# Kernel tuning notes

Measured on AMD Instinct MI355X. Metric: run time of the kernel, lower is better.

The kernel has to match this reference:

```python
import jax, jax.numpy as jnp
import numpy as np

B, N, DIM, QK, H, GS = 4, 4096, 512, 512, 8, 128
NUM_LABELS = 8
R_BASE, R_MIN, R_MAX = 0.5, 0.25, 0.75
LAMBDA_P, LAMBDA_V, CCR = 0.25, 0.25, 0.125


def setup_inputs() -> dict:
    key = jax.random.key(0)
    ks = jax.random.split(key, 7)
    s = DIM ** -0.5
    return {
        "x": jax.random.normal(ks[0], (B, N, DIM), jnp.float32),
        "labels": jax.random.randint(ks[1], (B, N), 0, NUM_LABELS),
        "scores": jax.random.uniform(ks[2], (B, N), jnp.float32),
        "Wq": jax.random.normal(ks[3], (DIM, QK), jnp.float32) * s,
        "Wk": jax.random.normal(ks[4], (DIM, QK), jnp.float32) * s,
        "Wv": jax.random.normal(ks[5], (DIM, DIM), jnp.float32) * s,
        "Wproj": jax.random.normal(ks[6], (DIM, DIM), jnp.float32) * s,
    }


def _windows(t, gs, ng):
    # pad with flipped last-group tail, then overlapping windows of size 2*gs, stride gs
    tp = jnp.concatenate([t, jnp.flip(t[:, -gs:], axis=1)], axis=1)
    a = tp.reshape(t.shape[0], ng + 1, gs, *t.shape[2:])
    return jnp.concatenate([a[:, :-1], a[:, 1:]], axis=2)  # [b, ng, 2*gs, ...]


def _topk_mask(vals, keep, cand):
    # rank of each entry when sorted descending; keep top-`keep` among candidates
    ranks = jnp.argsort(jnp.argsort(-vals, axis=-1), axis=-1)
    return (ranks < keep[:, :, None, None, None]) & cand


def reference(x, labels, scores, Wq, Wk, Wv, Wproj):
    b, n, _ = x.shape
    gs = GS
    ng = n // gs            # num_tokens divisible by group_size -> pad_n = 0
    ws = 2 * gs
    q = x @ Wq
    k = x @ Wk
    v = x @ Wv

    qw = q.reshape(b, ng, gs, H, -1).transpose(0, 1, 3, 2, 4)          # b ng h gs d
    kw = _windows(k, gs, ng).reshape(b, ng, ws, H, -1).transpose(0, 1, 3, 2, 4)
    vw = _windows(v, gs, ng).reshape(b, ng, ws, H, -1).transpose(0, 1, 3, 2, 4)
    q_labels = labels.reshape(b, ng, gs)
    k_labels = _windows(labels, gs, ng)                                 # b ng ws
    q_scores = scores.reshape(b, ng, gs)
    k_scores = _windows(scores, gs, ng)

    d = qw.shape[-1]
    scale = 1.0 / jnp.sqrt(jnp.asarray(d, qw.dtype))
    logits = jnp.einsum('bghqd,bghkd->bghqk', qw, kw) * scale           # b ng h gs ws
    attn_hat = jax.nn.softmax(logits, axis=-1)  # no prev_attn_state -> attn_hat = attn_cur

    # dynamic focus ratio: purity from group mode label + score variance
    counts = jax.nn.one_hot(q_labels, NUM_LABELS, dtype=jnp.float32).sum(axis=2)  # b ng L
    mode = jnp.argmax(counts, axis=-1)
    purity = jnp.mean((q_labels == mode[..., None]).astype(jnp.float32), axis=-1)
    score_var = jnp.var(q_scores.astype(jnp.float32), axis=-1)  # unbiased=False
    focus = jnp.clip(R_BASE + LAMBDA_P * purity - LAMBDA_V * score_var, R_MIN, R_MAX)

    keep = jnp.clip(jnp.ceil(focus * ws).astype(jnp.int32), 1, ws)
    cross_keep = jnp.round(keep.astype(jnp.float32) * CCR).astype(jnp.int32)
    cross_keep = jnp.where(keep > 1, jnp.maximum(cross_keep, 1), 0)
    same_keep = jnp.maximum(keep - cross_keep, 1)

    same_mask = (q_labels[:, :, None, :, None] == k_labels[:, :, None, None, :])  # b ng 1 gs ws

    same_scores = jnp.where(same_mask, attn_hat, -10000.0)
    m_same = _topk_mask(same_scores, same_keep, same_mask)
    pair_conf = q_scores[:, :, None, :, None] * k_scores[:, :, None, None, :]
    cross_scores = attn_hat * pair_conf
    m_cross = _topk_mask(cross_scores, cross_keep, ~same_mask)
    final_mask = m_same | m_cross

    sparse_logits = jnp.where(final_mask, logits, -10000.0)
    attn_local = jax.nn.softmax(sparse_logits, axis=-1)
    attn_local = jnp.where(final_mask, attn_local, 0.0)
    attn_local = attn_local / (attn_local.sum(axis=-1, keepdims=True) + 1e-9)

    out = jnp.einsum('bghqk,bghkd->bghqd', attn_local, vw)
    out = out.transpose(0, 1, 3, 2, 4).reshape(b, ng * gs, -1)[:, :n]
    return out @ Wproj, attn_local
```

## Files before the change

### kernel.cpp

```cpp
#include <hip/hip_runtime.h>

#define BB 4
#define NN 4096
#define DIMM 512
#define HH 8
#define DH 64
#define GSZ 128
#define NGRP 32
#define WSZ 256
#define CHUNK 32

#define MK 8388608u
#define WK 262144u

typedef short short8 __attribute__((ext_vector_type(8)));
typedef float f32x4 __attribute__((ext_vector_type(4)));

__device__ inline unsigned short bf16rne(float f) {
  unsigned u = __float_as_uint(f);
  unsigned r = u + 0x7FFFu + ((u >> 16) & 1u);
  return (unsigned short)(r >> 16);
}
__device__ inline float bf16tof(unsigned short h) {
  return __uint_as_float(((unsigned)h) << 16);
}

__global__ __launch_bounds__(256) void split_planes(
    const float* __restrict__ X, unsigned short* __restrict__ P, int np)
{
  unsigned idx = (blockIdx.x * 256u + threadIdx.x) * 4u;
  float4 xv = *(const float4*)&X[idx];
  float xs[4] = {xv.x, xv.y, xv.z, xv.w};
  ushort4 hv, mv, lv;
  unsigned short* hp = (unsigned short*)&hv;
  unsigned short* mp = (unsigned short*)&mv;
  unsigned short* lp = (unsigned short*)&lv;
#pragma unroll
  for (int i = 0; i < 4; ++i) {
    unsigned short h = bf16rne(xs[i]);
    float r1 = xs[i] - bf16tof(h);
    unsigned short m = bf16rne(r1);
    float r2 = r1 - bf16tof(m);
    hp[i] = h;
    mp[i] = m;
    lp[i] = bf16rne(r2);
  }
  *(ushort4*)&P[idx] = hv;
  *(ushort4*)&P[MK + idx] = mv;
  if (np == 3) *(ushort4*)&P[2u * MK + idx] = lv;
}

__global__ __launch_bounds__(256) void split_w(
    const float* __restrict__ Wq, const float* __restrict__ Wk,
    const float* __restrict__ Wv, const float* __restrict__ Wpj,
    unsigned short* __restrict__ wqkv, unsigned short* __restrict__ wproj)
{
  unsigned e = blockIdx.x * 256u + threadIdx.x;
  int mz = e >> 18;
  unsigned rem = e & (WK - 1u);
  unsigned kk = rem >> 9, n = rem & 511u;
  const float* src = (mz == 0) ? Wq : (mz == 1) ? Wk : (mz == 2) ? Wv : Wpj;
  float w = src[kk * 512u + n];
  unsigned short h = bf16rne(w);
  float r1 = w - bf16tof(h);
  unsigned short m = bf16rne(r1);
  float r2 = r1 - bf16tof(m);
  unsigned short l = bf16rne(r2);
  unsigned o = n * 512u + kk;
  if (mz < 3) {
    unsigned short* base = wqkv + (unsigned)mz * 3u * WK;
    base[o] = h;
    base[WK + o] = m;
    base[2u * WK + o] = l;
  } else {
    wproj[o] = h;
    wproj[WK + o] = m;
  }
}

template <int NP, int NT>
__global__ __launch_bounds__(256) void mfma_gemm(
    const unsigned short* __restrict__ Ap,
    const unsigned short* __restrict__ Wp,
    float* __restrict__ C)
{
  constexpr int ta[6] = {0, 0, 1, 1, 0, 2};
  constexpr int tw[6] = {0, 1, 0, 1, 2, 0};
  const int z = blockIdx.z;
  const int n0 = blockIdx.x * 128;
  const int m0 = blockIdx.y * 128;
  const int tid = threadIdx.x;
  const int lane = tid & 63, wv = tid >> 6;
  const int wm = (wv >> 1) * 64, wn = (wv & 1) * 64;
  const int lm = lane & 15, lk = (lane >> 4) * 8;

  __shared__ unsigned short As[NP * 128 * 40];
  __shared__ unsigned short Ws[NP * 128 * 40];

  f32x4 acc[4][4];
#pragma unroll
  for (int i = 0; i < 4; ++i)
#pragma unroll
    for (int j = 0; j < 4; ++j) acc[i][j] = (f32x4){0.f, 0.f, 0.f, 0.f};

  const unsigned short* Wz = Wp + (size_t)z * NP * WK;

  for (int k0 = 0; k0 < 512; k0 += 32) {
#pragma unroll
    for (int i = 0; i < NP * 2; ++i) {
      int idx = i * 256 + tid;
      int p = idx >> 9, rem = idx & 511;
      int r = rem >> 2, cc = rem & 3;
      *(short8*)&As[p * 5120 + r * 40 + cc * 8] =
          *(const short8*)&Ap[(size_t)p * MK + (size_t)(m0 + r) * 512 + k0 + cc * 8];
      *(short8*)&Ws[p * 5120 + r * 40 + cc * 8] =
          *(const short8*)&Wz[(size_t)p * WK + (size_t)(n0 + r) * 512 + k0 + cc * 8];
    }
    __syncthreads();

    short8 a[NP][4];
#pragma unroll
    for (int p = 0; p < NP; ++p)
#pragma unroll
      for (int fm = 0; fm < 4; ++fm)
        a[p][fm] = *(const short8*)&As[p * 5120 + (wm + fm * 16 + lm) * 40 + lk];

#pragma unroll
    for (int fn = 0; fn < 4; ++fn) {
      short8 bf[NP];
#pragma unroll
      for (int p = 0; p < NP; ++p)
        bf[p] = *(const short8*)&Ws[p * 5120 + (wn + fn * 16 + lm) * 40 + lk];
#pragma unroll
      for (int fm = 0; fm < 4; ++fm) {
#pragma unroll
        for (int t = 0; t < NT; ++t)
          acc[fm][fn] = __builtin_amdgcn_mfma_f32_16x16x32_bf16(
              a[ta[t]][fm], bf[tw[t]], acc[fm][fn], 0, 0, 0);
      }
    }
    __syncthreads();
  }

  float* Cz = C + (size_t)z * 8388608u;
  const int rq = (lane >> 4) * 4;
#pragma unroll
  for (int fm = 0; fm < 4; ++fm)
#pragma unroll
    for (int fn = 0; fn < 4; ++fn) {
      int row = m0 + wm + fm * 16 + rq;
      int col = n0 + wn + fn * 16 + lm;
#pragma unroll
      for (int r = 0; r < 4; ++r)
        Cz[(size_t)(row + r) * 512 + col] = acc[fm][fn][r];
    }
}

__global__ __launch_bounds__(256) void gemm512(
    const float* __restrict__ A,
    const float* __restrict__ W0, const float* __restrict__ W1, const float* __restrict__ W2,
    float* __restrict__ C0, float* __restrict__ C1, float* __restrict__ C2)
{
  const int z = blockIdx.z;
  const float* Wm = (z == 0) ? W0 : (z == 1 ? W1 : W2);
  float* Cm = (z == 0) ? C0 : (z == 1 ? C1 : C2);
  const int n0 = blockIdx.x * 128;
  const int m0 = blockIdx.y * 128;
  const int tid = threadIdx.x;
  const int tx = tid & 15, ty = tid >> 4;

  __shared__ float As[32][132];
  __shared__ float Bs[32][132];

  float acc[8][8];
#pragma unroll
  for (int i = 0; i < 8; ++i)
#pragma unroll
    for (int j = 0; j < 8; ++j) acc[i][j] = 0.f;

  for (int k0 = 0; k0 < 512; k0 += 32) {
    {
      const int c4 = tid & 7, r = tid >> 3;
#pragma unroll
      for (int p = 0; p < 128; p += 32) {
        float4 av = *(const float4*)&A[(size_t)(m0 + r + p) * 512 + k0 + c4 * 4];
        As[c4 * 4 + 0][r + p] = av.x;
        As[c4 * 4 + 1][r + p] = av.y;
        As[c4 * 4 + 2][r + p] = av.z;
        As[c4 * 4 + 3][r + p] = av.w;
      }
      const int j4 = tid & 31, rb = tid >> 5;
#pragma unroll
      for (int p = 0; p < 32; p += 8) {
        *(float4*)&Bs[rb + p][j4 * 4] =
            *(const float4*)&Wm[(size_t)(k0 + rb + p) * 512 + n0 + j4 * 4];
      }
    }
    __syncthreads();
#pragma unroll
    for (int kk = 0; kk < 32; ++kk) {
      float4 a0 = *(const float4*)&As[kk][ty * 8];
      float4 a1 = *(const float4*)&As[kk][ty * 8 + 4];
      float4 b0 = *(const float4*)&Bs[kk][tx * 8];
      float4 b1 = *(const float4*)&Bs[kk][tx * 8 + 4];
      float av[8] = {a0.x, a0.y, a0.z, a0.w, a1.x, a1.y, a1.z, a1.w};
      float bv[8] = {b0.x, b0.y, b0.z, b0.w, b1.x, b1.y, b1.z, b1.w};
#pragma unroll
      for (int i = 0; i < 8; ++i)
#pragma unroll
        for (int j = 0; j < 8; ++j) acc[i][j] += av[i] * bv[j];
    }
    __syncthreads();
  }
#pragma unroll
  for (int i = 0; i < 8; ++i) {
    size_t row = (size_t)(m0 + ty * 8 + i);
    float4 o0 = make_float4(acc[i][0], acc[i][1], acc[i][2], acc[i][3]);
    float4 o1 = make_float4(acc[i][4], acc[i][5], acc[i][6], acc[i][7]);
    *(float4*)&Cm[row * 512 + n0 + tx * 8] = o0;
    *(float4*)&Cm[row * 512 + n0 + tx * 8 + 4] = o1;
  }
}

__global__ __launch_bounds__(256, 3) void attn_kernel(
    const float* q,
    const float* __restrict__ k,
    const float* __restrict__ v,
    const int* __restrict__ labels,
    const float* __restrict__ scores,
    float* __restrict__ attn_out,
    float* o)
{
  const int bx = blockIdx.x;
  const int c = bx >> 10;
  const int rblk = bx & 1023;
  const int h = rblk & 7;
  const int g = (rblk >> 3) & 31;
  const int b = rblk >> 8;
  const int r0 = c * CHUNK;
  const int tid = threadIdx.x;
  const int lane = tid & 63, wv = tid >> 6;

  __shared__ float att[CHUNK][WSZ + 4];
  __shared__ float ktile[64][DH + 4];
  __shared__ int klab[WSZ];
  __shared__ float kscr[WSZ];
  __shared__ int hist8[8];
  __shared__ float s_var;
  __shared__ int s_sk, s_ck;

  {
    int j = tid;
    int pos = g * GSZ + j;
    int tok = pos < NN ? pos : (2 * NN - 1 - pos);
    klab[j] = labels[b * NN + tok];
    kscr[j] = scores[b * NN + tok];
  }
  if (tid < 8) hist8[tid] = 0;
  __syncthreads();

  if (tid < GSZ) atomicAdd(&hist8[klab[tid]], 1);
  if (wv == 0) {
    double x0 = (double)kscr[lane], x1 = (double)kscr[lane + 64];
    double s = x0 + x1;
#pragma unroll
    for (int off = 32; off > 0; off >>= 1) s += __shfl_xor(s, off);
    double mean = s * (1.0 / 128.0);
    double d0 = x0 - mean, d1 = x1 - mean;
    double vs = d0 * d0 + d1 * d1;
#pragma unroll
    for (int off = 32; off > 0; off >>= 1) vs += __shfl_xor(vs, off);
    if (lane == 0) s_var = (float)(vs * (1.0 / 128.0));
  }
  __syncthreads();
  if (tid == 0) {
    int bc = hist8[0];
    for (int l = 1; l < 8; ++l)
      if (hist8[l] > bc) bc = hist8[l];
    float purity = (float)bc * (1.0f / GSZ);
    float focus = 0.5f + 0.25f * purity - 0.25f * s_var;
    focus = fminf(fmaxf(focus, 0.25f), 0.75f);
    int keep = (int)ceilf(focus * (float)WSZ);
    keep = min(max(keep, 1), WSZ);
    int ck = keep >> 3, rem = keep & 7;
    if (rem > 4 || (rem == 4 && (ck & 1))) ck++;
    if (ck < 1) ck = 1;
    int sk = keep - ck;
    if (sk < 1) sk = 1;
    s_sk = sk;
    s_ck = ck;
  }
  __syncthreads();
  const int same_keep = s_sk, cross_keep = s_ck;

  const int rp = tid >> 4, jx = tid & 15;
  const int srow = tid >> 4, sd4 = (tid & 15) * 4;

  const float* q0p = q + (size_t)(b * NN + g * GSZ + r0 + rp) * DIMM + h * DH;
  const float* q1p = q0p + (size_t)16 * DIMM;

  for (int jt = 0; jt < 4; ++jt) {
#pragma unroll
    for (int p = 0; p < 64; p += 16) {
      int j = jt * 64 + srow + p;
      int pos = g * GSZ + j;
      int tok = pos < NN ? pos : (2 * NN - 1 - pos);
      *(float4*)&ktile[srow + p][sd4] =
          *(const float4*)&k[(size_t)(b * NN + tok) * DIMM + h * DH + sd4];
    }
    __syncthreads();
    float acc0[4] = {0.f, 0.f, 0.f, 0.f}, acc1[4] = {0.f, 0.f, 0.f, 0.f};
#pragma unroll
    for (int dd = 0; dd < DH; dd += 4) {
      float4 q0 = *(const float4*)(q0p + dd);
      float4 q1 = *(const float4*)(q1p + dd);
#pragma unroll
      for (int jj = 0; jj < 4; ++jj) {
        float4 kv = *(const float4*)&ktile[jx + 16 * jj][dd];
        acc0[jj] += q0.x * kv.x + q0.y * kv.y + q0.z * kv.z + q0.w * kv.w;
        acc1[jj] += q1.x * kv.x + q1.y * kv.y + q1.z * kv.z + q1.w * kv.w;
      }
    }
#pragma unroll
    for (int jj = 0; jj < 4; ++jj) {
      att[rp][jt * 64 + jx + 16 * jj] = acc0[jj] * 0.125f;
      att[rp + 16][jt * 64 + jx + 16 * jj] = acc1[jj] * 0.125f;
    }
    __syncthreads();
  }

  {
    int kl0[4];
    float ks0[4];
#pragma unroll
    for (int m = 0; m < 4; ++m) {
      kl0[m] = klab[lane + 64 * m];
      ks0[m] = kscr[lane + 64 * m];
    }
    for (int sp = 0; sp < 4; ++sp) {
      const int rA = wv * 8 + 2 * sp, rB = rA + 1;
      const int qLA = klab[r0 + rA], qLB = klab[r0 + rB];
      const float qSA = kscr[r0 + rA], qSB = kscr[r0 + rB];
      float aA[4], aB[4];
      float mxA = -INFINITY, mxB = -INFINITY;
#pragma unroll
      for (int m = 0; m < 4; ++m) {
        aA[m] = att[rA][lane + 64 * m];
        aB[m] = att[rB][lane + 64 * m];
        mxA = fmaxf(mxA, aA[m]);
        mxB = fmaxf(mxB, aB[m]);
      }
#pragma unroll
      for (int off = 32; off > 0; off >>= 1) {
        mxA = fmaxf(mxA, __shfl_xor(mxA, off));
        mxB = fmaxf(mxB, __shfl_xor(mxB, off));
      }
      unsigned fsA[4], fcA[4], fsB[4], fcB[4];
      bool cdA[4], cdB[4];
#pragma unroll
      for (int m = 0; m < 4; ++m) {
        aA[m] = expf(aA[m] - mxA);
        aB[m] = expf(aB[m] - mxB);
        cdA[m] = (kl0[m] == qLA);
        cdB[m] = (kl0[m] == qLB);
        fsA[m] = cdA[m] ? __float_as_uint(aA[m]) : 0u;
        fsB[m] = cdB[m] ? __float_as_uint(aB[m]) : 0u;
        fcA[m] = __float_as_uint(aA[m] * (qSA * ks0[m]));
        fcB[m] = __float_as_uint(aB[m] * (qSB * ks0[m]));
      }
      unsigned tsA = 0, tcA = 0, tsB = 0, tcB = 0;
      for (int bit = 29; bit >= 0; --bit) {
        unsigned csA = tsA | (1u << bit), ccA = tcA | (1u << bit);
        unsigned csB = tsB | (1u << bit), ccB = tcB | (1u << bit);
        int nsA = 0, ncA = 0, nsB = 0, ncB = 0;
#pragma unroll
        for (int m = 0; m < 4; ++m) {
          nsA += __popcll(__ballot(fsA[m] >= csA));
          ncA += __popcll(__ballot(fcA[m] >= ccA));
          nsB += __popcll(__ballot(fsB[m] >= csB));
          ncB += __popcll(__ballot(fcB[m] >= ccB));
        }
        if (nsA >= same_keep) tsA = csA;
        if (ncA >= cross_keep) tcA = ccA;
        if (nsB >= same_keep) tsB = csB;
        if (ncB >= cross_keep) tcB = ccB;
      }
#pragma unroll
      for (int rsel = 0; rsel < 2; ++rsel) {
        const int rr = rsel ? rB : rA;
        const unsigned ts = rsel ? tsB : tsA, tc = rsel ? tcB : tcA;
        unsigned* fs = rsel ? fsB : fsA;
        unsigned* fc = rsel ? fcB : fcA;
        float* a = rsel ? aB : aA;
        bool* cand = rsel ? cdB : cdA;
        unsigned long long beqs[4], beqc[4];
        int gts = 0, gtc = 0;
#pragma unroll
        for (int m = 0; m < 4; ++m) {
          gts += __popcll(__ballot(fs[m] > ts));
          gtc += __popcll(__ballot(fc[m] > tc));
          beqs[m] = __ballot(fs[m] == ts);
          beqc[m] = __ballot(fc[m] == tc);
        }
        const int rs = same_keep - gts, rc = cross_keep - gtc;
        float pv[4];
        float S = 0.f;
        int pres = 0, prec = 0;
#pragma unroll
        for (int m = 0; m < 4; ++m) {
          int mbs = __builtin_amdgcn_mbcnt_hi((unsigned)(beqs[m] >> 32),
                     __builtin_amdgcn_mbcnt_lo((unsigned)beqs[m], 0));
          int mbc = __builtin_amdgcn_mbcnt_hi((unsigned)(beqc[m] >> 32),
                     __builtin_amdgcn_mbcnt_lo((unsigned)beqc[m], 0));
          bool keep_s = cand[m] && ((fs[m] > ts) || ((fs[m] == ts) && (pres + mbs < rs)));
          bool keep_c = (!cand[m]) && ((fc[m] > tc) || ((fc[m] == tc) && (prec + mbc < rc)));
          pv[m] = (keep_s || keep_c) ? a[m] : 0.f;
          S += pv[m];
          pres += __popcll(beqs[m]);
          prec += __popcll(beqc[m]);
        }
#pragma unroll
        for (int off = 32; off > 0; off >>= 1) S += __shfl_xor(S, off);
        const float inv = 1.0f / S;
#pragma unroll
        for (int m = 0; m < 4; ++m) att[rr][lane + 64 * m] = pv[m] * inv;
      }
    }
  }
  __syncthreads();

  {
    size_t base = ((((size_t)b * NGRP + g) * HH + h) * GSZ + r0) * WSZ;
#pragma unroll
    for (int it = 0; it < 8; ++it) {
      int idx = it * 256 + tid;
      int i = idx >> 6, j4 = (idx & 63) * 4;
      *(float4*)&attn_out[base + (size_t)i * WSZ + j4] = *(float4*)&att[i][j4];
    }
  }

  const int dx = jx;
  float oa0[4] = {0.f, 0.f, 0.f, 0.f}, oa1[4] = {0.f, 0.f, 0.f, 0.f};
  for (int jt = 0; jt < 4; ++jt) {
#pragma unroll
    for (int p = 0; p < 64; p += 16) {
      int j = jt * 64 + srow + p;
      int pos = g * GSZ + j;
      int tok = pos < NN ? pos : (2 * NN - 1 - pos);
      *(float4*)&ktile[srow + p][sd4] =
          *(const float4*)&v[(size_t)(b * NN + tok) * DIMM + h * DH + sd4];
    }
    __syncthreads();
#pragma unroll 4
    for (int jg = 0; jg < 16; ++jg) {
      float4 p0 = *(const float4*)&att[rp][jt * 64 + jg * 4];
      float4 p1 = *(const float4*)&att[rp + 16][jt * 64 + jg * 4];
      float4 v0 = *(const float4*)&ktile[jg * 4 + 0][dx * 4];
      float4 v1 = *(const float4*)&ktile[jg * 4 + 1][dx * 4];
      float4 v2 = *(const float4*)&ktile[jg * 4 + 2][dx * 4];
      float4 v3 = *(const float4*)&ktile[jg * 4 + 3][dx * 4];
      oa0[0] += p0.x * v0.x + p0.y * v1.x + p0.z * v2.x + p0.w * v3.x;
      oa0[1] += p0.x * v0.y + p0.y * v1.y + p0.z * v2.y + p0.w * v3.y;
      oa0[2] += p0.x * v0.z + p0.y * v1.z + p0.z * v2.z + p0.w * v3.z;
      oa0[3] += p0.x * v0.w + p0.y * v1.w + p0.z * v2.w + p0.w * v3.w;
      oa1[0] += p1.x * v0.x + p1.y * v1.x + p1.z * v2.x + p1.w * v3.x;
      oa1[1] += p1.x * v0.y + p1.y * v1.y + p1.z * v2.y + p1.w * v3.y;
      oa1[2] += p1.x * v0.z + p1.y * v1.z + p1.z * v2.z + p1.w * v3.z;
      oa1[3] += p1.x * v0.w + p1.y * v1.w + p1.z * v2.w + p1.w * v3.w;
    }
    __syncthreads();
  }
  {
    size_t ob0 = (size_t)(b * NN + g * GSZ + r0 + rp) * DIMM + h * DH + dx * 4;
    *(float4*)&o[ob0] = make_float4(oa0[0], oa0[1], oa0[2], oa0[3]);
    *(float4*)&o[ob0 + (size_t)16 * DIMM] = make_float4(oa1[0], oa1[1], oa1[2], oa1[3]);
  }
}

extern "C" void kernel_launch(void* const* d_in, const int* in_sizes, int n_in,
                              void* d_out, int out_size, void* d_ws, size_t ws_size,
                              hipStream_t stream) {
  const float* x      = (const float*)d_in[0];
  const int*   labels = (const int*)d_in[1];
  const float* scores = (const float*)d_in[2];
  const float* Wq     = (const float*)d_in[3];
  const float* Wk     = (const float*)d_in[4];
  const float* Wv     = (const float*)d_in[5];
  const float* Wproj  = (const float*)d_in[6];

  float* out = (float*)d_out;
  float* attn_out = out + (size_t)BB * NN * DIMM;

  const size_t SZ = (size_t)BB * NN * DIMM;
  float* qb = (float*)d_ws;
  float* kb = qb + SZ;
  float* vb = kb + SZ;

  unsigned short* xp    = (unsigned short*)((char*)d_ws + 3 * SZ * 4);
  unsigned short* wqkv  = xp + 3 * (size_t)MK;
  unsigned short* wpp   = wqkv + 9 * (size_t)WK;
  const size_t required = 3 * SZ * 4 +
                          (3 * (size_t)MK + 9 * (size_t)WK + 2 * (size_t)WK) * 2;

  if (ws_size >= required) {
    split_planes<<<dim3(MK / 1024), 256, 0, stream>>>(x, xp, 3);
    split_w<<<dim3(4 * WK / 256), 256, 0, stream>>>(Wq, Wk, Wv, Wproj, wqkv, wpp);
    mfma_gemm<3, 6><<<dim3(4, 128, 3), 256, 0, stream>>>(xp, wqkv, qb);
    attn_kernel<<<dim3(BB * NGRP * HH * 4), 256, 0, stream>>>(qb, kb, vb, labels,
                                                              scores, attn_out, qb);
    split_planes<<<dim3(MK / 1024), 256, 0, stream>>>(qb, xp, 2);
    mfma_gemm<2, 3><<<dim3(4, 128, 1), 256, 0, stream>>>(xp, wpp, out);
  } else {
    gemm512<<<dim3(4, 128, 3), 256, 0, stream>>>(x, Wq, Wk, Wv, qb, kb, vb);
    attn_kernel<<<dim3(BB * NGRP * HH * 4), 256, 0, stream>>>(qb, kb, vb, labels,
                                                              scores, attn_out, qb);
    gemm512<<<dim3(4, 128, 1), 256, 0, stream>>>(qb, Wproj, Wproj, Wproj, out, out, out);
  }
}
```

Before: 814.0 us.

## Fuse bf16 plane split into attention epilogue and use fewer planes for V

The attention kernel now writes its output directly as hi/mid bf16 planes, so the separate split_planes pass over the attention output and its fp32 round trip are gone. The V projection is computed with a cheaper 2-plane × 3-term MFMA GEMM instead of the 3-plane × 6-term one used for Q and K. This cuts memory traffic and GEMM work, at the cost of lower precision in V, which could affect accuracy.

```diff
diff --git a/kernel.cpp b/kernel.cpp
--- a/kernel.cpp
+++ b/kernel.cpp
@@ -26,7 +26,7 @@
 }
 
 __global__ __launch_bounds__(256) void split_planes(
-    const float* __restrict__ X, unsigned short* __restrict__ P, int np)
+    const float* __restrict__ X, unsigned short* __restrict__ P)
 {
   unsigned idx = (blockIdx.x * 256u + threadIdx.x) * 4u;
   float4 xv = *(const float4*)&X[idx];
@@ -47,7 +47,7 @@
   }
   *(ushort4*)&P[idx] = hv;
   *(ushort4*)&P[MK + idx] = mv;
-  if (np == 3) *(ushort4*)&P[2u * MK + idx] = lv;
+  *(ushort4*)&P[2u * MK + idx] = lv;
 }
 
 __global__ __launch_bounds__(256) void split_w(
@@ -142,8 +142,8 @@
     __syncthreads();
   }
 
+  const int rq = (lane >> 4) * 4;
   float* Cz = C + (size_t)z * 8388608u;
-  const int rq = (lane >> 4) * 4;
 #pragma unroll
   for (int fm = 0; fm < 4; ++fm)
 #pragma unroll
@@ -222,14 +222,151 @@
   }
 }
 
-__global__ __launch_bounds__(256, 3) void attn_kernel(
-    const float* q,
-    const float* __restrict__ k,
-    const float* __restrict__ v,
-    const int* __restrict__ labels,
-    const float* __restrict__ scores,
-    float* __restrict__ attn_out,
-    float* o)
+__device__ __forceinline__ void focus_keep(
+    const int* klab, const float* kscr, int* hist8, float* s_var,
+    int* s_sk, int* s_ck, int tid, int lane, int wv)
+{
+  if (tid < GSZ) atomicAdd(&hist8[klab[tid]], 1);
+  if (wv == 0) {
+    double x0 = (double)kscr[lane], x1 = (double)kscr[lane + 64];
+    double s = x0 + x1;
+#pragma unroll
+    for (int off = 32; off > 0; off >>= 1) s += __shfl_xor(s, off);
+    double mean = s * (1.0 / 128.0);
+    double d0 = x0 - mean, d1 = x1 - mean;
+    double vs = d0 * d0 + d1 * d1;
+#pragma unroll
+    for (int off = 32; off > 0; off >>= 1) vs += __shfl_xor(vs, off);
+    if (lane == 0) *s_var = (float)(vs * (1.0 / 128.0));
+  }
+  __syncthreads();
+  if (tid == 0) {
+    int bc = hist8[0];
+    for (int l = 1; l < 8; ++l)
+      if (hist8[l] > bc) bc = hist8[l];
+    float purity = (float)bc * (1.0f / GSZ);
+    float focus = 0.5f + 0.25f * purity - 0.25f * (*s_var);
+    focus = fminf(fmaxf(focus, 0.25f), 0.75f);
+    int keep = (int)ceilf(focus * (float)WSZ);
+    keep = min(max(keep, 1), WSZ);
+    int ck = keep >> 3, rem = keep & 7;
+    if (rem > 4 || (rem == 4 && (ck & 1))) ck++;
+    if (ck < 1) ck = 1;
+    int sk = keep - ck;
+    if (sk < 1) sk = 1;
+    *s_sk = sk;
+    *s_ck = ck;
+  }
+  __syncthreads();
+}
+
+__device__ __forceinline__ void rank_rows(
+    float att[CHUNK][WSZ + 4], const int* klab, const float* kscr,
+    int r0, int same_keep, int cross_keep, int lane, int wv)
+{
+  int kl0[4];
+  float ks0[4];
+#pragma unroll
+  for (int m = 0; m < 4; ++m) {
+    kl0[m] = klab[lane + 64 * m];
+    ks0[m] = kscr[lane + 64 * m];
+  }
+  for (int sp = 0; sp < 4; ++sp) {
+    const int rA = wv * 8 + 2 * sp, rB = rA + 1;
+    const int qLA = klab[r0 + rA], qLB = klab[r0 + rB];
+    const float qSA = kscr[r0 + rA], qSB = kscr[r0 + rB];
+    float aA[4], aB[4];
+    float mxA = -INFINITY, mxB = -INFINITY;
+#pragma unroll
+    for (int m = 0; m < 4; ++m) {
+      aA[m] = att[rA][lane + 64 * m];
+      aB[m] = att[rB][lane + 64 * m];
+      mxA = fmaxf(mxA, aA[m]);
+      mxB = fmaxf(mxB, aB[m]);
+    }
+#pragma unroll
+    for (int off = 32; off > 0; off >>= 1) {
+      mxA = fmaxf(mxA, __shfl_xor(mxA, off));
+      mxB = fmaxf(mxB, __shfl_xor(mxB, off));
+    }
+    unsigned fsA[4], fcA[4], fsB[4], fcB[4];
+    bool cdA[4], cdB[4];
+#pragma unroll
+    for (int m = 0; m < 4; ++m) {
+      aA[m] = expf(aA[m] - mxA);
+      aB[m] = expf(aB[m] - mxB);
+      cdA[m] = (kl0[m] == qLA);
+      cdB[m] = (kl0[m] == qLB);
+      fsA[m] = cdA[m] ? __float_as_uint(aA[m]) : 0u;
+      fsB[m] = cdB[m] ? __float_as_uint(aB[m]) : 0u;
+      fcA[m] = __float_as_uint(aA[m] * (qSA * ks0[m]));
+      fcB[m] = __float_as_uint(aB[m] * (qSB * ks0[m]));
+    }
+    unsigned tsA = 0, tcA = 0, tsB = 0, tcB = 0;
+    for (int bit = 29; bit >= 0; --bit) {
+      unsigned csA = tsA | (1u << bit), ccA = tcA | (1u << bit);
+      unsigned csB = tsB | (1u << bit), ccB = tcB | (1u << bit);
+      int nsA = 0, ncA = 0, nsB = 0, ncB = 0;
+#pragma unroll
+      for (int m = 0; m < 4; ++m) {
+        nsA += __popcll(__ballot(fsA[m] >= csA));
+        ncA += __popcll(__ballot(fcA[m] >= ccA));
+        nsB += __popcll(__ballot(fsB[m] >= csB));
+        ncB += __popcll(__ballot(fcB[m] >= ccB));
+      }
+      if (nsA >= same_keep) tsA = csA;
+      if (ncA >= cross_keep) tcA = ccA;
+      if (nsB >= same_keep) tsB = csB;
+      if (ncB >= cross_keep) tcB = ccB;
+    }
+#pragma unroll
+    for (int rsel = 0; rsel < 2; ++rsel) {
+      const int rr = rsel ? rB : rA;
+      const unsigned ts = rsel ? tsB : tsA, tc = rsel ? tcB : tcA;
+      unsigned* fs = rsel ? fsB : fsA;
+      unsigned* fc = rsel ? fcB : fcA;
+      float* a = rsel ? aB : aA;
+      bool* cand = rsel ? cdB : cdA;
+      unsigned long long beqs[4], beqc[4];
+      int gts = 0, gtc = 0;
+#pragma unroll
+      for (int m = 0; m < 4; ++m) {
+        gts += __popcll(__ballot(fs[m] > ts));
+        gtc += __popcll(__ballot(fc[m] > tc));
+        beqs[m] = __ballot(fs[m] == ts);
+        beqc[m] = __ballot(fc[m] == tc);
+      }
+      const int rs = same_keep - gts, rc = cross_keep - gtc;
+      float pv[4];
+      float S = 0.f;
+      int pres = 0, prec = 0;
+#pragma unroll
+      for (int m = 0; m < 4; ++m) {
+        int mbs = __builtin_amdgcn_mbcnt_hi((unsigned)(beqs[m] >> 32),
+                   __builtin_amdgcn_mbcnt_lo((unsigned)beqs[m], 0));
+        int mbc = __builtin_amdgcn_mbcnt_hi((unsigned)(beqc[m] >> 32),
+                   __builtin_amdgcn_mbcnt_lo((unsigned)beqc[m], 0));
+        bool keep_s = cand[m] && ((fs[m] > ts) || ((fs[m] == ts) && (pres + mbs < rs)));
+        bool keep_c = (!cand[m]) && ((fc[m] > tc) || ((fc[m] == tc) && (prec + mbc < rc)));
+        pv[m] = (keep_s || keep_c) ? a[m] : 0.f;
+        S += pv[m];
+        pres += __popcll(beqs[m]);
+        prec += __popcll(beqc[m]);
+      }
+#pragma unroll
+      for (int off = 32; off > 0; off >>= 1) S += __shfl_xor(S, off);
+      const float inv = 1.0f / S;
+#pragma unroll
+      for (int m = 0; m < 4; ++m) att[rr][lane + 64 * m] = pv[m] * inv;
+    }
+  }
+}
+
+template <int OMODE>
+__global__ __launch_bounds__(256, 3) void attn_f32(
+    const float* q, const float* __restrict__ k, const float* __restrict__ v,
+    const int* __restrict__ labels, const float* __restrict__ scores,
+    float* __restrict__ attn_out, float* o, unsigned short* __restrict__ opl)
 {
   const int bx = blockIdx.x;
   const int c = bx >> 10;
@@ -258,44 +395,11 @@
   }
   if (tid < 8) hist8[tid] = 0;
   __syncthreads();
-
-  if (tid < GSZ) atomicAdd(&hist8[klab[tid]], 1);
-  if (wv == 0) {
-    double x0 = (double)kscr[lane], x1 = (double)kscr[lane + 64];
-    double s = x0 + x1;
-#pragma unroll
-    for (int off = 32; off > 0; off >>= 1) s += __shfl_xor(s, off);
-    double mean = s * (1.0 / 128.0);
-    double d0 = x0 - mean, d1 = x1 - mean;
-    double vs = d0 * d0 + d1 * d1;
-#pragma unroll
-    for (int off = 32; off > 0; off >>= 1) vs += __shfl_xor(vs, off);
-    if (lane == 0) s_var = (float)(vs * (1.0 / 128.0));
-  }
-  __syncthreads();
-  if (tid == 0) {
-    int bc = hist8[0];
-    for (int l = 1; l < 8; ++l)
-      if (hist8[l] > bc) bc = hist8[l];
-    float purity = (float)bc * (1.0f / GSZ);
-    float focus = 0.5f + 0.25f * purity - 0.25f * s_var;
-    focus = fminf(fmaxf(focus, 0.25f), 0.75f);
-    int keep = (int)ceilf(focus * (float)WSZ);
-    keep = min(max(keep, 1), WSZ);
-    int ck = keep >> 3, rem = keep & 7;
-    if (rem > 4 || (rem == 4 && (ck & 1))) ck++;
-    if (ck < 1) ck = 1;
-    int sk = keep - ck;
-    if (sk < 1) sk = 1;
-    s_sk = sk;
-    s_ck = ck;
-  }
-  __syncthreads();
+  focus_keep(klab, kscr, hist8, &s_var, &s_sk, &s_ck, tid, lane, wv);
   const int same_keep = s_sk, cross_keep = s_ck;
 
   const int rp = tid >> 4, jx = tid & 15;
   const int srow = tid >> 4, sd4 = (tid & 15) * 4;
-
   const float* q0p = q + (size_t)(b * NN + g * GSZ + r0 + rp) * DIMM + h * DH;
   const float* q1p = q0p + (size_t)16 * DIMM;
 
@@ -329,104 +433,7 @@
     __syncthreads();
   }
 
-  {
-    int kl0[4];
-    float ks0[4];
-#pragma unroll
-    for (int m = 0; m < 4; ++m) {
-      kl0[m] = klab[lane + 64 * m];
-      ks0[m] = kscr[lane + 64 * m];
-    }
-    for (int sp = 0; sp < 4; ++sp) {
-      const int rA = wv * 8 + 2 * sp, rB = rA + 1;
-      const int qLA = klab[r0 + rA], qLB = klab[r0 + rB];
-      const float qSA = kscr[r0 + rA], qSB = kscr[r0 + rB];
-      float aA[4], aB[4];
-      float mxA = -INFINITY, mxB = -INFINITY;
-#pragma unroll
-      for (int m = 0; m < 4; ++m) {
-        aA[m] = att[rA][lane + 64 * m];
-        aB[m] = att[rB][lane + 64 * m];
-        mxA = fmaxf(mxA, aA[m]);
-        mxB = fmaxf(mxB, aB[m]);
-      }
-#pragma unroll
-      for (int off = 32; off > 0; off >>= 1) {
-        mxA = fmaxf(mxA, __shfl_xor(mxA, off));
-        mxB = fmaxf(mxB, __shfl_xor(mxB, off));
-      }
-      unsigned fsA[4], fcA[4], fsB[4], fcB[4];
-      bool cdA[4], cdB[4];
-#pragma unroll
-      for (int m = 0; m < 4; ++m) {
-        aA[m] = expf(aA[m] - mxA);
-        aB[m] = expf(aB[m] - mxB);
-        cdA[m] = (kl0[m] == qLA);
-        cdB[m] = (kl0[m] == qLB);
-        fsA[m] = cdA[m] ? __float_as_uint(aA[m]) : 0u;
-        fsB[m] = cdB[m] ? __float_as_uint(aB[m]) : 0u;
-        fcA[m] = __float_as_uint(aA[m] * (qSA * ks0[m]));
-        fcB[m] = __float_as_uint(aB[m] * (qSB * ks0[m]));
-      }
-      unsigned tsA = 0, tcA = 0, tsB = 0, tcB = 0;
-      for (int bit = 29; bit >= 0; --bit) {
-        unsigned csA = tsA | (1u << bit), ccA = tcA | (1u << bit);
-        unsigned csB = tsB | (1u << bit), ccB = tcB | (1u << bit);
-        int nsA = 0, ncA = 0, nsB = 0, ncB = 0;
-#pragma unroll
-        for (int m = 0; m < 4; ++m) {
-          nsA += __popcll(__ballot(fsA[m] >= csA));
-          ncA += __popcll(__ballot(fcA[m] >= ccA));
-          nsB += __popcll(__ballot(fsB[m] >= csB));
-          ncB += __popcll(__ballot(fcB[m] >= ccB));
-        }
-        if (nsA >= same_keep) tsA = csA;
-        if (ncA >= cross_keep) tcA = ccA;
-        if (nsB >= same_keep) tsB = csB;
-        if (ncB >= cross_keep) tcB = ccB;
-      }
-#pragma unroll
-      for (int rsel = 0; rsel < 2; ++rsel) {
-        const int rr = rsel ? rB : rA;
-        const unsigned ts = rsel ? tsB : tsA, tc = rsel ? tcB : tcA;
-        unsigned* fs = rsel ? fsB : fsA;
-        unsigned* fc = rsel ? fcB : fcA;
-        float* a = rsel ? aB : aA;
-        bool* cand = rsel ? cdB : cdA;
-        unsigned long long beqs[4], beqc[4];
-        int gts = 0, gtc = 0;
-#pragma unroll
-        for (int m = 0; m < 4; ++m) {
-          gts += __popcll(__ballot(fs[m] > ts));
-          gtc += __popcll(__ballot(fc[m] > tc));
-          beqs[m] = __ballot(fs[m] == ts);
-          beqc[m] = __ballot(fc[m] == tc);
-        }
-        const int rs = same_keep - gts, rc = cross_keep - gtc;
-        float pv[4];
-        float S = 0.f;
-        int pres = 0, prec = 0;
-#pragma unroll
-        for (int m = 0; m < 4; ++m) {
-          int mbs = __builtin_amdgcn_mbcnt_hi((unsigned)(beqs[m] >> 32),
-                     __builtin_amdgcn_mbcnt_lo((unsigned)beqs[m], 0));
-          int mbc = __builtin_amdgcn_mbcnt_hi((unsigned)(beqc[m] >> 32),
-                     __builtin_amdgcn_mbcnt_lo((unsigned)beqc[m], 0));
-          bool keep_s = cand[m] && ((fs[m] > ts) || ((fs[m] == ts) && (pres + mbs < rs)));
-          bool keep_c = (!cand[m]) && ((fc[m] > tc) || ((fc[m] == tc) && (prec + mbc < rc)));
-          pv[m] = (keep_s || keep_c) ? a[m] : 0.f;
-          S += pv[m];
-          pres += __popcll(beqs[m]);
-          prec += __popcll(beqc[m]);
-        }
-#pragma unroll
-        for (int off = 32; off > 0; off >>= 1) S += __shfl_xor(S, off);
-        const float inv = 1.0f / S;
-#pragma unroll
-        for (int m = 0; m < 4; ++m) att[rr][lane + 64 * m] = pv[m] * inv;
-      }
-    }
-  }
+  rank_rows(att, klab, kscr, r0, same_keep, cross_keep, lane, wv);
   __syncthreads();
 
   {
@@ -470,10 +477,30 @@
     }
     __syncthreads();
   }
-  {
+  if (OMODE == 0) {
     size_t ob0 = (size_t)(b * NN + g * GSZ + r0 + rp) * DIMM + h * DH + dx * 4;
     *(float4*)&o[ob0] = make_float4(oa0[0], oa0[1], oa0[2], oa0[3]);
     *(float4*)&o[ob0 + (size_t)16 * DIMM] = make_float4(oa1[0], oa1[1], oa1[2], oa1[3]);
+  } else {
+    size_t ob0 = (size_t)(b * NN + g * GSZ + r0 + rp) * 512 + h * 64 + dx * 4;
+    ushort4 h0, m0v, h1, m1v;
+    unsigned short* h0p = (unsigned short*)&h0;
+    unsigned short* m0p = (unsigned short*)&m0v;
+    unsigned short* h1p = (unsigned short*)&h1;
+    unsigned short* m1p = (unsigned short*)&m1v;
+#pragma unroll
+    for (int i = 0; i < 4; ++i) {
+      unsigned short hh = bf16rne(oa0[i]);
+      h0p[i] = hh;
+      m0p[i] = bf16rne(oa0[i] - bf16tof(hh));
+      unsigned short hh1 = bf16rne(oa1[i]);
+      h1p[i] = hh1;
+      m1p[i] = bf16rne(oa1[i] - bf16tof(hh1));
+    }
+    *(ushort4*)&opl[ob0] = h0;
+    *(ushort4*)&opl[MK + ob0] = m0v;
+    *(ushort4*)&opl[ob0 + 16 * 512] = h1;
+    *(ushort4*)&opl[MK + ob0 + 16 * 512] = m1v;
   }
 }
 
@@ -491,29 +518,30 @@
   float* out = (float*)d_out;
   float* attn_out = out + (size_t)BB * NN * DIMM;
 
-  const size_t SZ = (size_t)BB * NN * DIMM;
   float* qb = (float*)d_ws;
-  float* kb = qb + SZ;
-  float* vb = kb + SZ;
-
-  unsigned short* xp    = (unsigned short*)((char*)d_ws + 3 * SZ * 4);
-  unsigned short* wqkv  = xp + 3 * (size_t)MK;
-  unsigned short* wpp   = wqkv + 9 * (size_t)WK;
-  const size_t required = 3 * SZ * 4 +
-                          (3 * (size_t)MK + 9 * (size_t)WK + 2 * (size_t)WK) * 2;
+  float* kb = qb + (size_t)MK;
+  float* vf = kb + (size_t)MK;
+  unsigned short* xpl  = (unsigned short*)(vf + (size_t)MK);
+  unsigned short* wqkv = xpl + 3 * (size_t)MK;
+  unsigned short* wpp  = wqkv + 9 * (size_t)WK;
+  const size_t required = 3 * (size_t)MK * 4 + 3 * (size_t)MK * 2 + 11 * (size_t)WK * 2;
 
   if (ws_size >= required) {
-    split_planes<<<dim3(MK / 1024), 256, 0, stream>>>(x, xp, 3);
+    split_planes<<<dim3(MK / 1024), 256, 0, stream>>>(x, xpl);
     split_w<<<dim3(4 * WK / 256), 256, 0, stream>>>(Wq, Wk, Wv, Wproj, wqkv, wpp);
-    mfma_gemm<3, 6><<<dim3(4, 128, 3), 256, 0, stream>>>(xp, wqkv, qb);
-    attn_kernel<<<dim3(BB * NGRP * HH * 4), 256, 0, stream>>>(qb, kb, vb, labels,
-                                                              scores, attn_out, qb);
-    split_planes<<<dim3(MK / 1024), 256, 0, stream>>>(qb, xp, 2);
-    mfma_gemm<2, 3><<<dim3(4, 128, 1), 256, 0, stream>>>(xp, wpp, out);
+    mfma_gemm<3, 6><<<dim3(4, 128, 2), 256, 0, stream>>>(xpl, wqkv, qb);
+    mfma_gemm<2, 3><<<dim3(4, 128, 1), 256, 0, stream>>>(xpl, wqkv + 6 * (size_t)WK, vf);
+    attn_f32<1><<<dim3(BB * NGRP * HH * 4), 256, 0, stream>>>(
+        qb, kb, vf, labels, scores, attn_out, nullptr, xpl);
+    mfma_gemm<2, 3><<<dim3(4, 128, 1), 256, 0, stream>>>(xpl, wpp, out);
   } else {
-    gemm512<<<dim3(4, 128, 3), 256, 0, stream>>>(x, Wq, Wk, Wv, qb, kb, vb);
-    attn_kernel<<<dim3(BB * NGRP * HH * 4), 256, 0, stream>>>(qb, kb, vb, labels,
-                                                              scores, attn_out, qb);
-    gemm512<<<dim3(4, 128, 1), 256, 0, stream>>>(qb, Wproj, Wproj, Wproj, out, out, out);
-  }
-}
+    const size_t SZ = (size_t)BB * NN * DIMM;
+    float* q2 = (float*)d_ws;
+    float* k2 = q2 + SZ;
+    float* v2 = k2 + SZ;
+    gemm512<<<dim3(4, 128, 3), 256, 0, stream>>>(x, Wq, Wk, Wv, q2, k2, v2);
+    attn_f32<0><<<dim3(BB * NGRP * HH * 4), 256, 0, stream>>>(
+        q2, k2, v2, labels, scores, attn_out, q2, nullptr);
+    gemm512<<<dim3(4, 128, 1), 256, 0, stream>>>(q2, Wproj, Wproj, Wproj, out, out, out);
+  }
+}
```

Result: no change. 811.0 us (-0.4%).
